# Kernel tuning notes

Hardware: AMD Instinct MI355X
Metric: run time of the kernel (lower is better)

The kernel has to match this reference:

```python
import jax, jax.numpy as jnp
import numpy as np

N, IN_DIM, OUT_DIM = 8192, 512, 256


def setup_inputs() -> dict:
    key = jax.random.key(0)
    k1, k2, k3 = jax.random.split(key, 3)
    X = jax.random.normal(k1, (N, IN_DIM), dtype=jnp.float32)
    # torch nn.Linear(in_dim, out_dim, bias=False): y = x @ W^T; store as [in_dim, out_dim]
    W = jax.random.normal(k2, (IN_DIM, OUT_DIM), dtype=jnp.float32) / np.sqrt(IN_DIM)
    # a: Linear(2*out_dim, 1, bias=False) -> vector of length 2*out_dim
    a = jax.random.normal(k3, (2 * OUT_DIM,), dtype=jnp.float32) / np.sqrt(2 * OUT_DIM)
    return {"X": X, "W": W, "a": a}


def reference(X, W, a):
    H = X @ W  # [N, D]
    D = H.shape[1]
    # a([Hi ; Hj]) = Hi @ a[:D] + Hj @ a[D:] -> avoid materializing [N,N,2D]
    e = (H @ a[:D])[:, None] + (H @ a[D:])[None, :]  # [N, N]
    e = jnp.where(e > 0, e, 0.2 * e)  # leaky_relu(0.2)
    A = jax.nn.softmax(e, axis=-1)  # row softmax [N, N]
    out = A @ H  # [N, D]
    return out, A
```

## Files before the change

### kernel.cpp

```cpp
#include <hip/hip_runtime.h>
#include <math.h>

#define NN 8192
#define KDIM 512
#define DD 256
#define CS 32
#define NC 256

typedef float4 f4;
typedef __attribute__((ext_vector_type(4))) float f4v;

__device__ __forceinline__ float dot4(const f4& x, const f4& y) {
  return x.x * y.x + x.y * y.y + x.z * y.z + x.w * y.w;
}

__global__ __launch_bounds__(256) void k_gemm(const float* __restrict__ X,
                                              const float* __restrict__ W,
                                              const float* __restrict__ av,
                                              float* __restrict__ H,
                                              float* __restrict__ s,
                                              float* __restrict__ t,
                                              float* __restrict__ Ctot1,
                                              float* __restrict__ cs1) {
  __shared__ float Xs[32][64];
  __shared__ float Ws[32][64];
  const int tid = threadIdx.x;
  const int tx = tid & 15;
  const int ty = tid >> 4;
  const int r0 = blockIdx.x * 64;
  const int c0 = blockIdx.y * 64;

  if (blockIdx.y == 1) {
    f4 z = {0.f, 0.f, 0.f, 0.f};
    *reinterpret_cast<f4*>(&Ctot1[blockIdx.x * 1024 + tid * 4]) = z;
  } else if (blockIdx.y == 2 && blockIdx.x == 0 && tid < 128) {
    f4 z = {0.f, 0.f, 0.f, 0.f};
    *reinterpret_cast<f4*>(&cs1[tid * 4]) = z;
  }

  float acc[4][4] = {};
  for (int k0 = 0; k0 < KDIM; k0 += 32) {
#pragma unroll
    for (int q = 0; q < 2; ++q) {
      int fi = tid + q * 256;
      int r = fi >> 3;
      int kq = fi & 7;
      f4 v = *reinterpret_cast<const f4*>(&X[(size_t)(r0 + r) * KDIM + k0 + kq * 4]);
      Xs[kq * 4 + 0][r] = v.x; Xs[kq * 4 + 1][r] = v.y;
      Xs[kq * 4 + 2][r] = v.z; Xs[kq * 4 + 3][r] = v.w;
    }
#pragma unroll
    for (int q = 0; q < 2; ++q) {
      int fi = tid + q * 256;
      int k = fi >> 4;
      int cq = fi & 15;
      *reinterpret_cast<f4*>(&Ws[k][cq * 4]) =
          *reinterpret_cast<const f4*>(&W[(size_t)(k0 + k) * DD + c0 + cq * 4]);
    }
    __syncthreads();
#pragma unroll
    for (int k = 0; k < 32; ++k) {
      f4 xv = *reinterpret_cast<const f4*>(&Xs[k][ty * 4]);
      f4 wv = *reinterpret_cast<const f4*>(&Ws[k][tx * 4]);
      float xs[4] = {xv.x, xv.y, xv.z, xv.w};
      float ws[4] = {wv.x, wv.y, wv.z, wv.w};
#pragma unroll
      for (int i = 0; i < 4; ++i)
#pragma unroll
        for (int j = 0; j < 4; ++j) acc[i][j] += xs[i] * ws[j];
    }
    __syncthreads();
  }
#pragma unroll
  for (int i = 0; i < 4; ++i) {
    f4 v = {acc[i][0], acc[i][1], acc[i][2], acc[i][3]};
    *reinterpret_cast<f4*>(&H[(size_t)(r0 + ty * 4 + i) * DD + c0 + tx * 4]) = v;
  }

  if (c0 == 0) {
    int wid = tid >> 6, lane = tid & 63;
    float* wv1 = &Xs[0][0];
    float* wv2 = &Xs[0][0] + 512;
    for (int k = tid; k < KDIM; k += 256) {
      float a1acc = 0.f, a2acc = 0.f;
#pragma unroll 8
      for (int d4 = 0; d4 < DD / 4; ++d4) {
        f4 wrow = *reinterpret_cast<const f4*>(&W[(size_t)k * DD + d4 * 4]);
        f4 a1v = *reinterpret_cast<const f4*>(&av[d4 * 4]);
        f4 a2v = *reinterpret_cast<const f4*>(&av[DD + d4 * 4]);
        a1acc += dot4(wrow, a1v);
        a2acc += dot4(wrow, a2v);
      }
      wv1[k] = a1acc;
      wv2[k] = a2acc;
    }
    __syncthreads();
    f4 w1a = *reinterpret_cast<const f4*>(&wv1[lane * 8]);
    f4 w1b = *reinterpret_cast<const f4*>(&wv1[lane * 8 + 4]);
    f4 w2a = *reinterpret_cast<const f4*>(&wv2[lane * 8]);
    f4 w2b = *reinterpret_cast<const f4*>(&wv2[lane * 8 + 4]);
    for (int rr = 0; rr < 16; ++rr) {
      int i = r0 + wid * 16 + rr;
      f4 xa = *reinterpret_cast<const f4*>(&X[(size_t)i * KDIM + lane * 8]);
      f4 xb = *reinterpret_cast<const f4*>(&X[(size_t)i * KDIM + lane * 8 + 4]);
      float p1 = dot4(xa, w1a) + dot4(xb, w1b);
      float p2 = dot4(xa, w2a) + dot4(xb, w2b);
      for (int off = 32; off > 0; off >>= 1) {
        p1 += __shfl_down(p1, off);
        p2 += __shfl_down(p2, off);
      }
      if (lane == 0) { s[i] = p1; t[i] = p2; }
    }
  }
}

__global__ __launch_bounds__(256) void k_mid(const float* __restrict__ s,
                                             const float* __restrict__ t,
                                             const float* __restrict__ H,
                                             float* __restrict__ E1,
                                             float* __restrict__ E2,
                                             float* __restrict__ c1,
                                             float* __restrict__ c2,
                                             int* __restrict__ perm,
                                             float* __restrict__ Es1,
                                             float* __restrict__ Es2,
                                             int* __restrict__ kidx,
                                             float* __restrict__ Ctot1,
                                             float* __restrict__ Ctot2,
                                             float* __restrict__ cs1,
                                             float* __restrict__ cs2) {
  __shared__ float lred[4];
  __shared__ int   kJ[16], kC[16];
  __shared__ float kE1[16], kE2[16];
  const int b = blockIdx.x, tid = threadIdx.x;
  const int wid = tid >> 6, lane = tid & 63;
  float m = -1e30f;
#pragma unroll
  for (int q = 0; q < 8; ++q) {
    int idx = (q * 256 + tid) * 4;
    f4 v = *reinterpret_cast<const f4*>(&t[idx]);
    m = fmaxf(m, fmaxf(fmaxf(v.x, v.y), fmaxf(v.z, v.w)));
  }
  for (int off = 32; off > 0; off >>= 1) m = fmaxf(m, __shfl_down(m, off));
  if (lane == 0) lred[wid] = m;
  __syncthreads();
  float tmax = fmaxf(fmaxf(lred[0], lred[1]), fmaxf(lred[2], lred[3]));

  if (tid < 16) {
    int i = b * 16 + tid;
    float ti = t[i];
    E1[i] = expf(ti);
    E2[i] = expf(0.2f * ti);
    float si = s[i];
    float e = si + tmax;
    float mm = e > 0.f ? e : 0.2f * e;
    c1[i] = expf(si - mm);
    c2[i] = expf(0.2f * si - mm);
  }

  float tkv[4], skv[4]; int jj[4], cnt[4], cntk[4];
#pragma unroll
  for (int q = 0; q < 4; ++q) {
    jj[q] = b * 16 + wid * 4 + q;
    tkv[q] = t[jj[q]];
    skv[q] = -s[jj[q]];
    cnt[q] = 0;
    cntk[q] = 0;
  }
  for (int m2 = 0; m2 < 32; ++m2) {
    int i4 = m2 * 64 + lane;
    f4 v = *reinterpret_cast<const f4*>(&t[i4 * 4]);
    int base = i4 * 4;
#pragma unroll
    for (int q = 0; q < 4; ++q) {
      cnt[q] += (v.x < tkv[q]) || (v.x == tkv[q] && base + 0 < jj[q]);
      cnt[q] += (v.y < tkv[q]) || (v.y == tkv[q] && base + 1 < jj[q]);
      cnt[q] += (v.z < tkv[q]) || (v.z == tkv[q] && base + 2 < jj[q]);
      cnt[q] += (v.w < tkv[q]) || (v.w == tkv[q] && base + 3 < jj[q]);
      cntk[q] += (v.x <= skv[q]) + (v.y <= skv[q]) + (v.z <= skv[q]) + (v.w <= skv[q]);
    }
  }
#pragma unroll
  for (int q = 0; q < 4; ++q) {
    int c = cnt[q], ck = cntk[q];
    for (int off = 32; off > 0; off >>= 1) {
      c += __shfl_down(c, off);
      ck += __shfl_down(ck, off);
    }
    if (lane == 0) {
      float e1 = expf(tkv[q]);
      float e2 = expf(0.2f * tkv[q]);
      perm[c] = jj[q];
      Es1[c] = e1;
      Es2[c] = e2;
      kidx[jj[q]] = ck;
      int cc = c >> 5;
      int idx = wid * 4 + q;
      kJ[idx] = jj[q]; kC[idx] = cc; kE1[idx] = e1; kE2[idx] = e2;
      atomicAdd(&cs1[cc], e1);
      atomicAdd(&cs2[cc], e2);
    }
  }
  __syncthreads();
#pragma unroll
  for (int q = 0; q < 16; ++q) {
    int j = kJ[q], cc = kC[q];
    float h = H[(size_t)j * DD + tid];
    atomicAdd(&Ctot1[cc * DD + tid], kE1[q] * h);
    atomicAdd(&Ctot2[cc * DD + tid], kE2[q] * h);
  }
}

__global__ __launch_bounds__(256) void k_scan(const float* __restrict__ Ctot1,
                                              const float* __restrict__ Ctot2,
                                              const float* __restrict__ cs1,
                                              const float* __restrict__ cs2,
                                              const float* __restrict__ Es1,
                                              const float* __restrict__ Es2,
                                              const int* __restrict__ kidx,
                                              const float* __restrict__ c1,
                                              const float* __restrict__ c2,
                                              float* __restrict__ Cpre1,
                                              float* __restrict__ Cpre2,
                                              float* __restrict__ f1,
                                              float* __restrict__ f2) {
  __shared__ float sc1[NC], sc2[NC];
  const int c = blockIdx.x;
  const int d = threadIdx.x;
  float r1a = 0.f, r1b = 0.f, r2a = 0.f, r2b = 0.f;
  int cc = 0;
  for (; cc + 4 <= c; cc += 4) {
    r1a += Ctot1[(cc + 0) * DD + d];
    r1b += Ctot1[(cc + 1) * DD + d];
    r1a += Ctot1[(cc + 2) * DD + d];
    r1b += Ctot1[(cc + 3) * DD + d];
    r2a += Ctot2[(cc + 0) * DD + d];
    r2b += Ctot2[(cc + 1) * DD + d];
    r2a += Ctot2[(cc + 2) * DD + d];
    r2b += Ctot2[(cc + 3) * DD + d];
  }
  for (; cc < c; ++cc) {
    r1a += Ctot1[cc * DD + d];
    r2a += Ctot2[cc * DD + d];
  }
  float r1 = r1a + r1b, r2 = r2a + r2b;
  Cpre1[(size_t)c * DD + d] = r1;
  Cpre2[(size_t)c * DD + d] = r2;
  if (c == NC - 1) {
    Cpre1[(size_t)NC * DD + d] = r1 + Ctot1[c * DD + d];
    Cpre2[(size_t)NC * DD + d] = r2 + Ctot2[c * DD + d];
  }
  sc1[d] = cs1[d];
  sc2[d] = cs2[d];
  __syncthreads();
  for (int off = 1; off < NC; off <<= 1) {
    float y1 = (d >= off) ? sc1[d - off] : 0.f;
    float y2 = (d >= off) ? sc2[d - off] : 0.f;
    __syncthreads();
    sc1[d] += y1; sc2[d] += y2;
    __syncthreads();
  }
  if (d < 32) {
    int i = c * 32 + d;
    int ki = kidx[i];
    int ci = ki >> 5;
    float sp1 = ci ? sc1[ci - 1] : 0.f;
    float sp2 = ci ? sc2[ci - 1] : 0.f;
    for (int m = ci * CS; m < ki; ++m) { sp1 += Es1[m]; sp2 += Es2[m]; }
    float T1s = sc1[NC - 1];
    float a1 = c1[i], a2 = c2[i];
    float Z = a1 * (T1s - sp1) + a2 * sp2;
    float rZ = 1.0f / Z;
    f1[i] = rZ * a1;
    f2[i] = rZ * a2;
  }
}

__global__ __launch_bounds__(256) void k_finstream(const int* __restrict__ kidx,
                                                   const float* __restrict__ Es1,
                                                   const float* __restrict__ Es2,
                                                   const int* __restrict__ perm,
                                                   const float* __restrict__ H,
                                                   const float* __restrict__ Cpre1,
                                                   const float* __restrict__ Cpre2,
                                                   const float* __restrict__ f1,
                                                   const float* __restrict__ f2,
                                                   float* __restrict__ out,
                                                   const float* __restrict__ s,
                                                   const float* __restrict__ t,
                                                   const float* __restrict__ E1,
                                                   const float* __restrict__ E2,
                                                   float* __restrict__ A) {
  const int bb = blockIdx.x;
  const int d = threadIdx.x;
  {
    float T1 = Cpre1[(size_t)NC * DD + d];
#pragma unroll
    for (int r = 0; r < 4; ++r) {
      int i = bb * 4 + r;
      int ki = kidx[i];
      int ci = ki >> 5;
      float P1 = Cpre1[(size_t)ci * DD + d];
      float P2 = Cpre2[(size_t)ci * DD + d];
      for (int m = ci * CS; m < ki; ++m) {
        float h = H[(size_t)perm[m] * DD + d];
        P1 += Es1[m] * h;
        P2 += Es2[m] * h;
      }
      out[(size_t)i * DD + d] = f1[i] * (T1 - P1) + f2[i] * P2;
    }
  }
  {
    int i0 = (bb >> 3) * 32;
    int j0 = (bb & 7) * 1024 + d * 4;
    f4 t4  = *reinterpret_cast<const f4*>(&t[j0]);
    f4 e14 = *reinterpret_cast<const f4*>(&E1[j0]);
    f4 e24 = *reinterpret_cast<const f4*>(&E2[j0]);
#pragma unroll 4
    for (int rr = 0; rr < 32; ++rr) {
      int i = i0 + rr;
      float ss = s[i], ff1 = f1[i], ff2 = f2[i];
      f4v o;
      float e;
      e = ss + t4.x; o.x = (e > 0.f) ? ff1 * e14.x : ff2 * e24.x;
      e = ss + t4.y; o.y = (e > 0.f) ? ff1 * e14.y : ff2 * e24.y;
      e = ss + t4.z; o.z = (e > 0.f) ? ff1 * e14.z : ff2 * e24.z;
      e = ss + t4.w; o.w = (e > 0.f) ? ff1 * e14.w : ff2 * e24.w;
      __builtin_nontemporal_store(o, reinterpret_cast<f4v*>(&A[(size_t)i * NN + j0]));
    }
  }
}

extern "C" void kernel_launch(void* const* d_in, const int* in_sizes, int n_in,
                              void* d_out, int out_size, void* d_ws, size_t ws_size,
                              hipStream_t stream) {
  const float* X  = (const float*)d_in[0];
  const float* W  = (const float*)d_in[1];
  const float* av = (const float*)d_in[2];
  float* outp = (float*)d_out;
  float* A = outp + (size_t)NN * DD;
  float* wsp = (float*)d_ws;

  float* s     = wsp + 0;
  float* t     = wsp + 8192;
  float* E1    = wsp + 16384;
  float* E2    = wsp + 24576;
  float* c1    = wsp + 32768;
  float* c2    = wsp + 40960;
  float* f1    = wsp + 49152;
  float* f2    = wsp + 57344;
  float* Ctot1 = wsp + 65536;
  float* Ctot2 = wsp + 131072;
  float* Cpre1 = wsp + 196608;
  float* Cpre2 = wsp + 262400;
  float* cs1   = wsp + 328192;
  float* cs2   = wsp + 328448;
  float* Es1   = wsp + 328704;
  float* Es2   = wsp + 336896;
  int*   kidx  = (int*)(wsp + 345088);
  int*   perm  = (int*)(wsp + 353280);
  float* H     = wsp + 393216;

  k_gemm<<<dim3(NN / 64, DD / 64), 256, 0, stream>>>(X, W, av, H, s, t, Ctot1, cs1);
  k_mid<<<NN / 16, 256, 0, stream>>>(s, t, H, E1, E2, c1, c2, perm, Es1, Es2,
                                     kidx, Ctot1, Ctot2, cs1, cs2);
  k_scan<<<NC, 256, 0, stream>>>(Ctot1, Ctot2, cs1, cs2, Es1, Es2, kidx, c1, c2,
                                 Cpre1, Cpre2, f1, f2);
  k_finstream<<<NN / 4, 256, 0, stream>>>(kidx, Es1, Es2, perm, H, Cpre1, Cpre2,
                                          f1, f2, outp, s, t, E1, E2, A);
}
```

Baseline: 202.6 us.

## Replace atomic chunk accumulation with dedicated chunk-sum kernel and enlarge GEMM tile

The sorted-chunk sums of exp-weighted H rows are no longer built in k_mid with global atomics. A new k_chunk kernel now gathers each chunk's 32 permuted rows and reduces them directly, which also removes the zero-initialisation inside the GEMM. The GEMM block tile grows from 64x64 to 128x64, with 8x4 outputs per thread, to raise arithmetic intensity. The cost is one extra kernel launch and higher register use per GEMM thread.

```diff
diff --git a/kernel.cpp b/kernel.cpp
--- a/kernel.cpp
+++ b/kernel.cpp
@@ -6,6 +6,8 @@
 #define DD 256
 #define CS 32
 #define NC 256
+#define BM 128
+#define BN 64
 
 typedef float4 f4;
 typedef __attribute__((ext_vector_type(4))) float f4v;
@@ -19,29 +21,18 @@
                                               const float* __restrict__ av,
                                               float* __restrict__ H,
                                               float* __restrict__ s,
-                                              float* __restrict__ t,
-                                              float* __restrict__ Ctot1,
-                                              float* __restrict__ cs1) {
-  __shared__ float Xs[32][64];
-  __shared__ float Ws[32][64];
+                                              float* __restrict__ t) {
+  __shared__ float Xs[32][BM];
+  __shared__ float Ws[32][BN];
   const int tid = threadIdx.x;
   const int tx = tid & 15;
   const int ty = tid >> 4;
-  const int r0 = blockIdx.x * 64;
-  const int c0 = blockIdx.y * 64;
-
-  if (blockIdx.y == 1) {
-    f4 z = {0.f, 0.f, 0.f, 0.f};
-    *reinterpret_cast<f4*>(&Ctot1[blockIdx.x * 1024 + tid * 4]) = z;
-  } else if (blockIdx.y == 2 && blockIdx.x == 0 && tid < 128) {
-    f4 z = {0.f, 0.f, 0.f, 0.f};
-    *reinterpret_cast<f4*>(&cs1[tid * 4]) = z;
-  }
-
-  float acc[4][4] = {};
+  const int r0 = blockIdx.x * BM;
+  const int c0 = blockIdx.y * BN;
+  float acc[8][4] = {};
   for (int k0 = 0; k0 < KDIM; k0 += 32) {
 #pragma unroll
-    for (int q = 0; q < 2; ++q) {
+    for (int q = 0; q < 4; ++q) {
       int fi = tid + q * 256;
       int r = fi >> 3;
       int kq = fi & 7;
@@ -60,21 +51,22 @@
     __syncthreads();
 #pragma unroll
     for (int k = 0; k < 32; ++k) {
-      f4 xv = *reinterpret_cast<const f4*>(&Xs[k][ty * 4]);
+      f4 xa = *reinterpret_cast<const f4*>(&Xs[k][ty * 8]);
+      f4 xb = *reinterpret_cast<const f4*>(&Xs[k][ty * 8 + 4]);
       f4 wv = *reinterpret_cast<const f4*>(&Ws[k][tx * 4]);
-      float xs[4] = {xv.x, xv.y, xv.z, xv.w};
+      float xs[8] = {xa.x, xa.y, xa.z, xa.w, xb.x, xb.y, xb.z, xb.w};
       float ws[4] = {wv.x, wv.y, wv.z, wv.w};
 #pragma unroll
-      for (int i = 0; i < 4; ++i)
+      for (int i = 0; i < 8; ++i)
 #pragma unroll
         for (int j = 0; j < 4; ++j) acc[i][j] += xs[i] * ws[j];
     }
     __syncthreads();
   }
 #pragma unroll
-  for (int i = 0; i < 4; ++i) {
+  for (int i = 0; i < 8; ++i) {
     f4 v = {acc[i][0], acc[i][1], acc[i][2], acc[i][3]};
-    *reinterpret_cast<f4*>(&H[(size_t)(r0 + ty * 4 + i) * DD + c0 + tx * 4]) = v;
+    *reinterpret_cast<f4*>(&H[(size_t)(r0 + ty * 8 + i) * DD + c0 + tx * 4]) = v;
   }
 
   if (c0 == 0) {
@@ -99,8 +91,8 @@
     f4 w1b = *reinterpret_cast<const f4*>(&wv1[lane * 8 + 4]);
     f4 w2a = *reinterpret_cast<const f4*>(&wv2[lane * 8]);
     f4 w2b = *reinterpret_cast<const f4*>(&wv2[lane * 8 + 4]);
-    for (int rr = 0; rr < 16; ++rr) {
-      int i = r0 + wid * 16 + rr;
+    for (int rr = 0; rr < 32; ++rr) {
+      int i = r0 + wid * 32 + rr;
       f4 xa = *reinterpret_cast<const f4*>(&X[(size_t)i * KDIM + lane * 8]);
       f4 xb = *reinterpret_cast<const f4*>(&X[(size_t)i * KDIM + lane * 8 + 4]);
       float p1 = dot4(xa, w1a) + dot4(xb, w1b);
@@ -116,7 +108,6 @@
 
 __global__ __launch_bounds__(256) void k_mid(const float* __restrict__ s,
                                              const float* __restrict__ t,
-                                             const float* __restrict__ H,
                                              float* __restrict__ E1,
                                              float* __restrict__ E2,
                                              float* __restrict__ c1,
@@ -124,14 +115,8 @@
                                              int* __restrict__ perm,
                                              float* __restrict__ Es1,
                                              float* __restrict__ Es2,
-                                             int* __restrict__ kidx,
-                                             float* __restrict__ Ctot1,
-                                             float* __restrict__ Ctot2,
-                                             float* __restrict__ cs1,
-                                             float* __restrict__ cs2) {
+                                             int* __restrict__ kidx) {
   __shared__ float lred[4];
-  __shared__ int   kJ[16], kC[16];
-  __shared__ float kE1[16], kE2[16];
   const int b = blockIdx.x, tid = threadIdx.x;
   const int wid = tid >> 6, lane = tid & 63;
   float m = -1e30f;
@@ -188,27 +173,39 @@
       ck += __shfl_down(ck, off);
     }
     if (lane == 0) {
-      float e1 = expf(tkv[q]);
-      float e2 = expf(0.2f * tkv[q]);
       perm[c] = jj[q];
-      Es1[c] = e1;
-      Es2[c] = e2;
+      Es1[c] = expf(tkv[q]);
+      Es2[c] = expf(0.2f * tkv[q]);
       kidx[jj[q]] = ck;
-      int cc = c >> 5;
-      int idx = wid * 4 + q;
-      kJ[idx] = jj[q]; kC[idx] = cc; kE1[idx] = e1; kE2[idx] = e2;
-      atomicAdd(&cs1[cc], e1);
-      atomicAdd(&cs2[cc], e2);
-    }
-  }
+    }
+  }
+}
+
+__global__ __launch_bounds__(256) void k_chunk(const float* __restrict__ H,
+                                               const float* __restrict__ Es1,
+                                               const float* __restrict__ Es2,
+                                               const int* __restrict__ perm,
+                                               float* __restrict__ Ctot1,
+                                               float* __restrict__ Ctot2,
+                                               float* __restrict__ cs1,
+                                               float* __restrict__ cs2) {
+  __shared__ int pms[CS];
+  int c = blockIdx.x;
+  int d = threadIdx.x;
+  if (d < CS) pms[d] = perm[c * CS + d];
   __syncthreads();
-#pragma unroll
-  for (int q = 0; q < 16; ++q) {
-    int j = kJ[q], cc = kC[q];
-    float h = H[(size_t)j * DD + tid];
-    atomicAdd(&Ctot1[cc * DD + tid], kE1[q] * h);
-    atomicAdd(&Ctot2[cc * DD + tid], kE2[q] * h);
-  }
+  float s1 = 0.f, s2 = 0.f, a1 = 0.f, a2 = 0.f;
+#pragma unroll 4
+  for (int kk = 0; kk < CS; ++kk) {
+    int mI = c * CS + kk;
+    float e1 = Es1[mI], e2 = Es2[mI];
+    float h = H[(size_t)pms[kk] * DD + d];
+    s1 += e1 * h; s2 += e2 * h;
+    a1 += e1;     a2 += e2;
+  }
+  Ctot1[c * DD + d] = s1;
+  Ctot2[c * DD + d] = s2;
+  if (d == 0) { cs1[c] = a1; cs2[c] = a2; }
 }
 
 __global__ __launch_bounds__(256) void k_scan(const float* __restrict__ Ctot1,
@@ -361,9 +358,9 @@
   int*   perm  = (int*)(wsp + 353280);
   float* H     = wsp + 393216;
 
-  k_gemm<<<dim3(NN / 64, DD / 64), 256, 0, stream>>>(X, W, av, H, s, t, Ctot1, cs1);
-  k_mid<<<NN / 16, 256, 0, stream>>>(s, t, H, E1, E2, c1, c2, perm, Es1, Es2,
-                                     kidx, Ctot1, Ctot2, cs1, cs2);
+  k_gemm<<<dim3(NN / BM, DD / BN), 256, 0, stream>>>(X, W, av, H, s, t);
+  k_mid<<<NN / 16, 256, 0, stream>>>(s, t, E1, E2, c1, c2, perm, Es1, Es2, kidx);
+  k_chunk<<<NC, 256, 0, stream>>>(H, Es1, Es2, perm, Ctot1, Ctot2, cs1, cs2);
   k_scan<<<NC, 256, 0, stream>>>(Ctot1, Ctot2, cs1, cs2, Es1, Es2, kidx, c1, c2,
                                  Cpre1, Cpre2, f1, f2);
   k_finstream<<<NN / 4, 256, 0, stream>>>(kidx, Es1, Es2, perm, H, Cpre1, Cpre2,
```

After: 212.3 us. 4.7% more time.
